# Performance work log

Measured on AMD Instinct MI355X. Metric: run time of the kernel, lower is better.

Reference implementation:

```python
import jax, jax.numpy as jnp
import numpy as np
from jax import lax

# ---- constants matching init_kwargs ----
NY, NX = 1024, 1024
DX, DY = 50.0, 50.0
TTOT = 32.0
DTMAX = 0.5
RHO, G, FD = 910.0, 9.81, 1e-17
EPS = 1e-10
T_FREQ = 5.0
N_STEPS = 64            # fixed step count (>= TTOT/DTMAX); dt masked to 0 once time >= TTOT
LAPSE = 0.0065          # degC per m elevation lapse rate (SMB model)
MELT_FACTOR = 0.5       # m ice / (degC * yr) ablation factor (SMB model)


def update_smb(Z_surf, precip, T_ma_lowest, T_mj_lowest, ice_mask):
    # Lapse-rate temperatures at the surface
    T_ma = T_ma_lowest - LAPSE * Z_surf   # mean annual temperature
    T_mj = T_mj_lowest - LAPSE * Z_surf   # mean July temperature
    accumulation = precip * (T_ma < 0.0).astype(Z_surf.dtype)
    ablation = MELT_FACTOR * jnp.maximum(T_mj, 0.0)
    return (accumulation - ablation) * ice_mask


def setup_inputs() -> dict:
    key = jax.random.key(0)
    k1, k2, k3 = jax.random.split(key, 3)
    # smooth mountain topography: 2500 m gaussian massif + small noise
    y = np.arange(NY, dtype=np.float32) * DY
    x = np.arange(NX, dtype=np.float32) * DX
    yy, xx = np.meshgrid(y, x, indexing="ij")
    cy, cx = y.mean(), x.mean()
    sigma = 0.25 * NX * DX
    z = 2500.0 * np.exp(-((yy - cy) ** 2 + (xx - cx) ** 2) / (2.0 * sigma ** 2))
    Z_topo = jnp.asarray(z, dtype=jnp.float32) + 5.0 * jax.random.normal(k1, (NY, NX), dtype=jnp.float32)
    precip_tensor = 2.0 * jax.random.uniform(k2, (NY, NX), dtype=jnp.float32)  # m ice / yr
    T_ma_lowest = jnp.float32(8.0) + jax.random.normal(k3, (), dtype=jnp.float32)
    T_mj_lowest = T_ma_lowest + jnp.float32(8.0)
    ice_mask = jnp.ones((NY, NX), dtype=jnp.float32)
    return {"precip_tensor": precip_tensor, "T_ma_lowest": T_ma_lowest,
            "T_mj_lowest": T_mj_lowest, "Z_topo": Z_topo, "ice_mask": ice_mask}


def _glacier_step(carry, _, Z_topo, precip, T_ma_lowest, T_mj_lowest, ice_mask):
    H_ice, Z_surf, smb, time, t_last = carry
    # staggered-grid averages and slopes (SIA diffusion)
    H_avg = 0.25 * (H_ice[:-1, :-1] + H_ice[1:, 1:] + H_ice[:-1, 1:] + H_ice[1:, :-1])
    Sx = (Z_surf[:, 1:] - Z_surf[:, :-1]) / DX
    Sy = (Z_surf[1:, :] - Z_surf[:-1, :]) / DY
    Sx = 0.5 * (Sx[:-1, :] + Sx[1:, :])          # (NY-1, NX-1)
    Sy = 0.5 * (Sy[:, :-1] + Sy[:, 1:])          # (NY-1, NX-1)
    Snorm = jnp.sqrt(Sx ** 2 + Sy ** 2 + EPS)
    D = FD * (RHO * G) ** 3 * H_avg ** 5 * Snorm ** 2 + EPS
    # adaptive CFL dt; torch uses .item() so dt is a non-differentiable constant
    dt = jnp.minimum(min(DX, DY) ** 2 / (2.7 * jnp.max(D)), DTMAX)
    dt = lax.stop_gradient(dt)
    dt = jnp.where(time < TTOT, dt, 0.0)         # freeze once ttot is reached
    qx = -(0.5 * (D[:-1, :] + D[1:, :])) * (Z_surf[1:-1, 1:] - Z_surf[1:-1, :-1]) / DX
    qy = -(0.5 * (D[:, :-1] + D[:, 1:])) * (Z_surf[1:, 1:-1] - Z_surf[:-1, 1:-1]) / DY
    dHdt = -(jnp.diff(qx, axis=1) / DX + jnp.diff(qy, axis=0) / DY)  # (NY-2, NX-2)
    H_new = H_ice.at[1:-1, 1:-1].add(dt * (dHdt + smb[1:-1, 1:-1]))
    H_new = jnp.maximum(H_new, 0.0)
    Z_new = Z_topo + H_new
    time = time + dt
    # refresh SMB every T_FREQ model years
    do_upd = (time - t_last) >= T_FREQ
    smb_new = update_smb(Z_new, precip, T_ma_lowest, T_mj_lowest, ice_mask)
    smb = jnp.where(do_upd, smb_new, smb)
    t_last = jnp.where(do_upd, time, t_last)
    return (H_new, Z_new, smb, time, t_last), None


def reference(precip_tensor, T_ma_lowest, T_mj_lowest, Z_topo, ice_mask):
    H_ice = jnp.zeros((NY, NX), dtype=jnp.float32)
    Z_surf = Z_topo + H_ice
    smb = update_smb(Z_surf, precip_tensor, T_ma_lowest, T_mj_lowest, ice_mask)
    time = jnp.float32(0.0)
    t_last = jnp.float32(0.0)
    step = lambda c, x: _glacier_step(c, x, Z_topo, precip_tensor, T_ma_lowest, T_mj_lowest, ice_mask)
    (H_ice, _, _, _, _), _ = lax.scan(step, (H_ice, Z_surf, smb, time, t_last), None, length=N_STEPS)
    return H_ice
```

## Files before the change

kernel.cpp:

```cpp
#include <hip/hip_runtime.h>
#include <math.h>

#define NYg 1024
#define NXg 1024
#define W   1024
#define NSTEPS 64
#define NBLK 256
#define EN (NBLK * W)

#define WS_SLOTS 0
#define WS_NBF   24576
#define WS_CTRL_END 32768
#define WS_GRIDS 32768

constexpr float DXf   = 50.0f;
constexpr float DYf   = 50.0f;
constexpr float TTOTf = 32.0f;
constexpr float DTMAXf= 0.5f;
constexpr float EPSf  = 1e-10f;
constexpr float TFREQ = 5.0f;
constexpr float LAPSE = 0.0065f;
constexpr float MELTF = 0.5f;
constexpr double RHOG = 910.0 * 9.81;
constexpr float  CDf  = (float)(1e-17 * RHOG * RHOG * RHOG);

__device__ __forceinline__ float scloadf(const float* p) {
    return __hip_atomic_load(p, __ATOMIC_RELAXED, __HIP_MEMORY_SCOPE_SYSTEM);
}
__device__ __forceinline__ void scstoref(float* p, float v) {
    __hip_atomic_store(p, v, __ATOMIC_RELAXED, __HIP_MEMORY_SCOPE_SYSTEM);
}
__device__ __forceinline__ unsigned scloadu(const unsigned* p) {
    return __hip_atomic_load(p, __ATOMIC_RELAXED, __HIP_MEMORY_SCOPE_SYSTEM);
}

__device__ __forceinline__ float dfunc(float h00, float h01, float h10, float h11,
                                       float z00, float z01, float z10, float z11)
{
    float havg = 0.25f * (h00 + h11 + h01 + h10);
    float sx = ((z01 - z00) + (z11 - z10)) * (0.5f / DXf);
    float sy = ((z10 - z00) + (z11 - z01)) * (0.5f / DYf);
    float sn = sqrtf(sx * sx + sy * sy + EPSf);
    float h2 = havg * havg;
    float h4 = h2 * h2;
    return CDf * (h4 * havg) * (sn * sn) + EPSf;
}

__global__ __launch_bounds__(256) void k_init(unsigned* __restrict__ ctrl)
{
    int idx = blockIdx.x * blockDim.x + threadIdx.x;
    int stride = gridDim.x * blockDim.x;
    for (int i = idx; i < WS_CTRL_END; i += stride) {
        unsigned v = 0u;
        if (i < NBLK) v = __float_as_uint(EPSf);
        ctrl[i] = v;
    }
}

__global__ __launch_bounds__(1024, 1) void k_run(
    float* __restrict__ EZa0, float* __restrict__ EZa1,
    float* __restrict__ EZb0, float* __restrict__ EZb1,
    float* __restrict__ EDa0, float* __restrict__ EDa1,
    float* __restrict__ EDb0, float* __restrict__ EDb1,
    const float* __restrict__ ztopo, const float* __restrict__ precip,
    const float* __restrict__ mask, const float* __restrict__ tma,
    const float* __restrict__ tmj, unsigned* __restrict__ ctrl,
    float* __restrict__ Hout)
{
    __shared__ float sZ[5][W];
    __shared__ float sH[5][W];
    __shared__ float sD[4][W];
    __shared__ float smax16[16];
    __shared__ float smax4[4];

    float*    slotsf = (float*)ctrl;
    unsigned* nbf    = ctrl + WS_NBF;

    const int c   = threadIdx.x;
    const int b   = blockIdx.x;
    const int r0  = b * 4;
    const int lane = c & 63, wid = c >> 6;
    const bool hasA = (b > 0), hasB = (b < NBLK - 1);
    const bool cL = (c >= 1), cR = (c <= NXg - 2);
    const int cm = (c == 0) ? 0 : c - 1;
    const int cp = (c == W - 1) ? W - 1 : c + 1;

    const float TMA = tma[0], TMJ = tmj[0];

    float z_[7];
    float h_[5];
    float dreg[4];
    float dtop, dtopL;
    float dbot, dbotL;
    float smbr[5], ztr[5];

    #pragma unroll
    for (int q = 0; q < 7; ++q) {
        int r = r0 - 1 + q;
        z_[q] = (r >= 0 && r < NYg) ? ztopo[r * W + c] : 0.0f;
    }
    #pragma unroll
    for (int rr = 0; rr < 5; ++rr) {
        int r = r0 + rr;
        h_[rr] = 0.0f;
        if (r < NYg) {
            float z = z_[rr + 1];
            ztr[rr] = z;
            float t_ma = TMA - LAPSE * z;
            float t_mj = TMJ - LAPSE * z;
            float acc  = (t_ma < 0.0f) ? precip[r * W + c] : 0.0f;
            float abl  = MELTF * fmaxf(t_mj, 0.0f);
            smbr[rr] = (acc - abl) * mask[r * W + c];
            sZ[rr][c] = z;
            sH[rr][c] = 0.0f;
        } else {
            ztr[rr] = 0.0f; smbr[rr] = 0.0f;
            sZ[rr][c] = 0.0f;
            sH[rr][c] = 0.0f;
        }
    }
    dtop = EPSf; dtopL = EPSf; dbot = EPSf; dbotL = EPSf;
    #pragma unroll
    for (int q = 0; q < 4; ++q) { dreg[q] = EPSf; sD[q][c] = EPSf; }
    __syncthreads();

    float t = 0.0f, tl = 0.0f;

    for (int s = 0; s < NSTEPS; ++s) {
        const float* EZar = (s & 1) ? EZa1 : EZa0;
        float*       EZaw = (s & 1) ? EZa0 : EZa1;
        const float* EZbr = (s & 1) ? EZb1 : EZb0;
        float*       EZbw = (s & 1) ? EZb0 : EZb1;
        const float* EDar = (s & 1) ? EDa1 : EDa0;
        float*       EDaw = (s & 1) ? EDa0 : EDa1;
        const float* EDbr = (s & 1) ? EDb1 : EDb0;
        float*       EDbw = (s & 1) ? EDb0 : EDb1;

        if (s > 0) {
            if (hasA)
                while (scloadu(&nbf[(b - 1) * 32]) < (unsigned)s) __builtin_amdgcn_s_sleep(1);
            if (hasB)
                while (scloadu(&nbf[(b + 1) * 32]) < (unsigned)s) __builtin_amdgcn_s_sleep(1);
            if (hasA) {
                z_[0] = scloadf(EZbr + (b - 1) * W + c);
                if (cR) dtop  = scloadf(EDbr + (b - 1) * W + c);
                if (cL) dtopL = scloadf(EDbr + (b - 1) * W + (c-1));
            }
            if (hasB) {
                z_[6] = scloadf(EZar + (b + 1) * W + c);
                if (cR) dbot  = scloadf(EDar + (b + 1) * W + c);
                if (cL) dbotL = scloadf(EDar + (b + 1) * W + (c-1));
            }
        }

        float dl[6], doa[6];
        dl[0] = dtopL;      doa[0] = dtop;
        dl[1] = sD[0][cm];  doa[1] = dreg[0];
        dl[2] = sD[1][cm];  doa[2] = dreg[1];
        dl[3] = sD[2][cm];  doa[3] = dreg[2];
        dl[4] = sD[3][cm];  doa[4] = dreg[3];
        dl[5] = dbotL;      doa[5] = dbot;

        float zl[5], zr[5];
        #pragma unroll
        for (int q = 0; q < 5; ++q) { zl[q] = sZ[q][cm]; zr[q] = sZ[q][cp]; }

        float qy[6];
        #pragma unroll
        for (int k = 0; k < 6; ++k)
            qy[k] = -0.5f * (dl[k] + doa[k]) * (z_[k + 1] - z_[k]) * (1.0f / DYf);

        float dh[5];
        bool  inter[5];
        #pragma unroll
        for (int rr = 0; rr < 5; ++rr) {
            int r = r0 + rr;
            bool iv = (r >= 1 && r <= NYg - 2 && cL && cR);
            float zc  = z_[rr + 1];
            float qxR = -0.5f * (doa[rr] + doa[rr + 1]) * (zr[rr] - zc) * (1.0f / DXf);
            float qxL = -0.5f * (dl[rr]  + dl[rr + 1])  * (zc - zl[rr]) * (1.0f / DXf);
            float d = -((qxR - qxL) * (1.0f / DXf) + (qy[rr + 1] - qy[rr]) * (1.0f / DYf));
            dh[rr] = iv ? d : 0.0f;
            inter[rr] = iv;
        }

        if (c < NBLK) {
            const float* sl = slotsf + s * NBLK + c;
            float v = scloadf(sl);
            while (__float_as_uint(v) == 0u) { __builtin_amdgcn_s_sleep(1); v = scloadf(sl); }
            #pragma unroll
            for (int off = 32; off >= 1; off >>= 1)
                v = fmaxf(v, __shfl_xor(v, off, 64));
            if (lane == 0) smax4[wid] = v;
        }
        __syncthreads();

        float mD = fmaxf(fmaxf(smax4[0], smax4[1]), fmaxf(smax4[2], smax4[3]));
        float dt = fminf(2500.0f / (2.7f * mD), DTMAXf);
        if (!(t < TTOTf)) dt = 0.0f;
        float nt  = t + dt;
        bool  upd = (nt - tl) >= TFREQ;

        #pragma unroll
        for (int rr = 0; rr < 5; ++rr) {
            int r = r0 + rr;
            if (r < NYg) {
                float h, z;
                if (inter[rr]) { h = fmaxf(h_[rr] + dt * (dh[rr] + smbr[rr]), 0.0f);
                                 z = ztr[rr] + h; }
                else           { h = 0.0f; z = z_[rr + 1]; }
                h_[rr] = h; z_[rr + 1] = z;
                sZ[rr][c] = z;
                sH[rr][c] = h;
                if (rr == 1 && hasA) scstoref(EZaw + b * W + c, z);
                if (rr == 3 && hasB) scstoref(EZbw + b * W + c, z);
                if (upd) {
                    float t_ma = TMA - LAPSE * z;
                    float t_mj = TMJ - LAPSE * z;
                    float acc  = (t_ma < 0.0f) ? precip[r * W + c] : 0.0f;
                    float abl  = MELTF * fmaxf(t_mj, 0.0f);
                    smbr[rr] = (acc - abl) * mask[r * W + c];
                }
            } else {
                h_[rr] = 0.0f;
            }
        }
        __syncthreads();

        if (s < NSTEPS - 1) {
            float m = 0.0f;
            float dv[4];
            #pragma unroll
            for (int rr = 0; rr < 4; ++rr) {
                int i = r0 + rr;
                float dd = 0.0f;
                if (i <= NYg - 2 && cR) {
                    dd = dfunc(h_[rr], sH[rr][c + 1],
                               h_[rr + 1], sH[rr + 1][c + 1],
                               z_[rr + 1], sZ[rr][c + 1],
                               z_[rr + 2], sZ[rr + 1][c + 1]);
                    m = fmaxf(m, dd);
                    if (rr == 0 && hasA) scstoref(EDaw + b * W + c, dd);
                    if (rr == 3 && hasB) scstoref(EDbw + b * W + c, dd);
                }
                dv[rr] = dd;
            }
            sD[0][c] = dv[0];
            sD[1][c] = dv[1];
            sD[2][c] = dv[2];
            sD[3][c] = dv[3];
            dreg[0] = dv[0]; dreg[1] = dv[1]; dreg[2] = dv[2]; dreg[3] = dv[3];
            #pragma unroll
            for (int off = 32; off >= 1; off >>= 1)
                m = fmaxf(m, __shfl_xor(m, off, 64));
            if (lane == 0) smax16[wid] = m;
            __syncthreads();
            if (c == 0) {
                #pragma unroll
                for (int q = 1; q < 16; ++q) m = fmaxf(m, smax16[q]);
                scstoref(slotsf + (s + 1) * NBLK + b, m);
            }
            asm volatile("s_waitcnt vmcnt(0)" ::: "memory");
            __syncthreads();
            if (c == 0)
                __hip_atomic_store(&nbf[b * 32], (unsigned)(s + 1),
                                   __ATOMIC_RELAXED, __HIP_MEMORY_SCOPE_SYSTEM);
        }

        t = nt;
        if (upd) tl = nt;
    }

    #pragma unroll
    for (int rr = 0; rr < 4; ++rr)
        Hout[(r0 + rr) * W + c] = h_[rr];
}

extern "C" void kernel_launch(void* const* d_in, const int* in_sizes, int n_in,
                              void* d_out, int out_size, void* d_ws, size_t ws_size,
                              hipStream_t stream)
{
    const float* precip = (const float*)d_in[0];
    const float* tma    = (const float*)d_in[1];
    const float* tmj    = (const float*)d_in[2];
    const float* ztopo  = (const float*)d_in[3];
    const float* mask   = (const float*)d_in[4];

    unsigned* ctrl = (unsigned*)d_ws;
    float* g = (float*)d_ws + WS_GRIDS;
    float* EZa0 = g + 0 * EN; float* EZa1 = g + 1 * EN;
    float* EZb0 = g + 2 * EN; float* EZb1 = g + 3 * EN;
    float* EDa0 = g + 4 * EN; float* EDa1 = g + 5 * EN;
    float* EDb0 = g + 6 * EN; float* EDb1 = g + 7 * EN;

    k_init<<<dim3(64), dim3(256), 0, stream>>>(ctrl);

    k_run<<<dim3(256), dim3(1024), 0, stream>>>(EZa0, EZa1, EZb0, EZb1,
                                                EDa0, EDa1, EDb0, EDb1,
                                                ztopo, precip, mask, tma, tmj,
                                                ctrl, (float*)d_out);
}
```

Measured before the change: 392.6 us.

## Speculate dt equals DTMAX to overlap update with global max reduction wait

Each step now computes the H/Z update and the next diffusivity using a guessed dt (DTMAX, or zero past TTOT) before waiting on the cross-block max slots. Once the true dt is known, it recomputes only if the guess was wrong, then commits state and publishes the block max. This hides the spin-wait latency behind useful work when the CFL limit is not active. It costs extra registers and duplicated code, and a full recompute on mispredicted steps.

```diff
diff --git a/kernel.cpp b/kernel.cpp
--- a/kernel.cpp
+++ b/kernel.cpp
@@ -184,49 +184,30 @@
             inter[rr] = iv;
         }
 
-        if (c < NBLK) {
-            const float* sl = slotsf + s * NBLK + c;
-            float v = scloadf(sl);
-            while (__float_as_uint(v) == 0u) { __builtin_amdgcn_s_sleep(1); v = scloadf(sl); }
-            #pragma unroll
-            for (int off = 32; off >= 1; off >>= 1)
-                v = fmaxf(v, __shfl_xor(v, off, 64));
-            if (lane == 0) smax4[wid] = v;
-        }
         __syncthreads();
 
-        float mD = fmaxf(fmaxf(smax4[0], smax4[1]), fmaxf(smax4[2], smax4[3]));
-        float dt = fminf(2500.0f / (2.7f * mD), DTMAXf);
-        if (!(t < TTOTf)) dt = 0.0f;
-        float nt  = t + dt;
-        bool  upd = (nt - tl) >= TFREQ;
-
+        const float dtg = (t < TTOTf) ? DTMAXf : 0.0f;
+        float hs[5], zs[5];
         #pragma unroll
         for (int rr = 0; rr < 5; ++rr) {
             int r = r0 + rr;
             if (r < NYg) {
                 float h, z;
-                if (inter[rr]) { h = fmaxf(h_[rr] + dt * (dh[rr] + smbr[rr]), 0.0f);
+                if (inter[rr]) { h = fmaxf(h_[rr] + dtg * (dh[rr] + smbr[rr]), 0.0f);
                                  z = ztr[rr] + h; }
                 else           { h = 0.0f; z = z_[rr + 1]; }
-                h_[rr] = h; z_[rr + 1] = z;
+                hs[rr] = h; zs[rr] = z;
                 sZ[rr][c] = z;
                 sH[rr][c] = h;
                 if (rr == 1 && hasA) scstoref(EZaw + b * W + c, z);
                 if (rr == 3 && hasB) scstoref(EZbw + b * W + c, z);
-                if (upd) {
-                    float t_ma = TMA - LAPSE * z;
-                    float t_mj = TMJ - LAPSE * z;
-                    float acc  = (t_ma < 0.0f) ? precip[r * W + c] : 0.0f;
-                    float abl  = MELTF * fmaxf(t_mj, 0.0f);
-                    smbr[rr] = (acc - abl) * mask[r * W + c];
-                }
             } else {
-                h_[rr] = 0.0f;
+                hs[rr] = 0.0f; zs[rr] = z_[rr + 1];
             }
         }
         __syncthreads();
 
+        float m16 = 0.0f;
         if (s < NSTEPS - 1) {
             float m = 0.0f;
             float dv[4];
@@ -235,10 +216,10 @@
                 int i = r0 + rr;
                 float dd = 0.0f;
                 if (i <= NYg - 2 && cR) {
-                    dd = dfunc(h_[rr], sH[rr][c + 1],
-                               h_[rr + 1], sH[rr + 1][c + 1],
-                               z_[rr + 1], sZ[rr][c + 1],
-                               z_[rr + 2], sZ[rr + 1][c + 1]);
+                    dd = dfunc(hs[rr], sH[rr][c + 1],
+                               hs[rr + 1], sH[rr + 1][c + 1],
+                               zs[rr], sZ[rr][c + 1],
+                               zs[rr + 1], sZ[rr + 1][c + 1]);
                     m = fmaxf(m, dd);
                     if (rr == 0 && hasA) scstoref(EDaw + b * W + c, dd);
                     if (rr == 3 && hasB) scstoref(EDbw + b * W + c, dd);
@@ -258,8 +239,98 @@
             if (c == 0) {
                 #pragma unroll
                 for (int q = 1; q < 16; ++q) m = fmaxf(m, smax16[q]);
-                scstoref(slotsf + (s + 1) * NBLK + b, m);
-            }
+                m16 = m;
+            }
+        }
+
+        if (c < NBLK) {
+            const float* sl = slotsf + s * NBLK + c;
+            float v = scloadf(sl);
+            while (__float_as_uint(v) == 0u) { __builtin_amdgcn_s_sleep(1); v = scloadf(sl); }
+            #pragma unroll
+            for (int off = 32; off >= 1; off >>= 1)
+                v = fmaxf(v, __shfl_xor(v, off, 64));
+            if (lane == 0) smax4[wid] = v;
+        }
+        __syncthreads();
+
+        float mD = fmaxf(fmaxf(smax4[0], smax4[1]), fmaxf(smax4[2], smax4[3]));
+        float dt = fminf(2500.0f / (2.7f * mD), DTMAXf);
+        if (!(t < TTOTf)) dt = 0.0f;
+
+        if (__float_as_uint(dt) != __float_as_uint(dtg)) {
+            #pragma unroll
+            for (int rr = 0; rr < 5; ++rr) {
+                int r = r0 + rr;
+                if (r < NYg) {
+                    float h, z;
+                    if (inter[rr]) { h = fmaxf(h_[rr] + dt * (dh[rr] + smbr[rr]), 0.0f);
+                                     z = ztr[rr] + h; }
+                    else           { h = 0.0f; z = z_[rr + 1]; }
+                    hs[rr] = h; zs[rr] = z;
+                    sZ[rr][c] = z;
+                    sH[rr][c] = h;
+                    if (rr == 1 && hasA) scstoref(EZaw + b * W + c, z);
+                    if (rr == 3 && hasB) scstoref(EZbw + b * W + c, z);
+                }
+            }
+            __syncthreads();
+            if (s < NSTEPS - 1) {
+                float m = 0.0f;
+                float dv[4];
+                #pragma unroll
+                for (int rr = 0; rr < 4; ++rr) {
+                    int i = r0 + rr;
+                    float dd = 0.0f;
+                    if (i <= NYg - 2 && cR) {
+                        dd = dfunc(hs[rr], sH[rr][c + 1],
+                                   hs[rr + 1], sH[rr + 1][c + 1],
+                                   zs[rr], sZ[rr][c + 1],
+                                   zs[rr + 1], sZ[rr + 1][c + 1]);
+                        m = fmaxf(m, dd);
+                        if (rr == 0 && hasA) scstoref(EDaw + b * W + c, dd);
+                        if (rr == 3 && hasB) scstoref(EDbw + b * W + c, dd);
+                    }
+                    dv[rr] = dd;
+                }
+                sD[0][c] = dv[0];
+                sD[1][c] = dv[1];
+                sD[2][c] = dv[2];
+                sD[3][c] = dv[3];
+                dreg[0] = dv[0]; dreg[1] = dv[1]; dreg[2] = dv[2]; dreg[3] = dv[3];
+                #pragma unroll
+                for (int off = 32; off >= 1; off >>= 1)
+                    m = fmaxf(m, __shfl_xor(m, off, 64));
+                if (lane == 0) smax16[wid] = m;
+                __syncthreads();
+                if (c == 0) {
+                    #pragma unroll
+                    for (int q = 1; q < 16; ++q) m = fmaxf(m, smax16[q]);
+                    m16 = m;
+                }
+            }
+        }
+
+        float nt  = t + dt;
+        bool  upd = (nt - tl) >= TFREQ;
+        #pragma unroll
+        for (int rr = 0; rr < 5; ++rr) {
+            h_[rr] = hs[rr];
+            z_[rr + 1] = zs[rr];
+            int r = r0 + rr;
+            if (upd && r < NYg) {
+                float z = zs[rr];
+                float t_ma = TMA - LAPSE * z;
+                float t_mj = TMJ - LAPSE * z;
+                float acc  = (t_ma < 0.0f) ? precip[r * W + c] : 0.0f;
+                float abl  = MELTF * fmaxf(t_mj, 0.0f);
+                smbr[rr] = (acc - abl) * mask[r * W + c];
+            }
+        }
+
+        if (s < NSTEPS - 1) {
+            if (c == 0)
+                scstoref(slotsf + (s + 1) * NBLK + b, m16);
             asm volatile("s_waitcnt vmcnt(0)" ::: "memory");
             __syncthreads();
             if (c == 0)
```

Result: no change. 393.3 us (+0.2%).

## Split grid into 512 persistent blocks of two rows each

Applied to the files above, without the earlier changes.

The persistent stencil kernel now uses 512 blocks that each own two rows, instead of 256 blocks owning four rows. The aim is two co-resident blocks per CU, which doubles wave occupancy for latency hiding and halves per-block work on each step's critical path. Halo exchange now uses one shared Z-row buffer plus separate up and down D buffers, and the global max reduction reads 512 slots. In exchange it relies on all 512 blocks being resident at once, because of the spin-wait neighbour flags. The launch bound of 8 also tightens the register budget, which may cause spills.

```diff
diff --git a/kernel.cpp b/kernel.cpp
--- a/kernel.cpp
+++ b/kernel.cpp
@@ -5,13 +5,12 @@
 #define NXg 1024
 #define W   1024
 #define NSTEPS 64
-#define NBLK 256
+#define NBLK 512
 #define EN (NBLK * W)
 
-#define WS_SLOTS 0
-#define WS_NBF   24576
-#define WS_CTRL_END 32768
-#define WS_GRIDS 32768
+#define WS_NBF   33280
+#define WS_CTRL_END 49664
+#define WS_GRIDS 65536
 
 constexpr float DXf   = 50.0f;
 constexpr float DYf   = 50.0f;
@@ -57,28 +56,27 @@
     }
 }
 
-__global__ __launch_bounds__(1024, 1) void k_run(
-    float* __restrict__ EZa0, float* __restrict__ EZa1,
-    float* __restrict__ EZb0, float* __restrict__ EZb1,
-    float* __restrict__ EDa0, float* __restrict__ EDa1,
-    float* __restrict__ EDb0, float* __restrict__ EDb1,
+__global__ __launch_bounds__(1024, 8) void k_run(
+    float* __restrict__ EZ0,  float* __restrict__ EZ1,
+    float* __restrict__ EDd0, float* __restrict__ EDd1,
+    float* __restrict__ EDu0, float* __restrict__ EDu1,
     const float* __restrict__ ztopo, const float* __restrict__ precip,
     const float* __restrict__ mask, const float* __restrict__ tma,
     const float* __restrict__ tmj, unsigned* __restrict__ ctrl,
     float* __restrict__ Hout)
 {
-    __shared__ float sZ[5][W];
-    __shared__ float sH[5][W];
-    __shared__ float sD[4][W];
+    __shared__ float sZ[3][W];
+    __shared__ float sH[3][W];
+    __shared__ float sD[2][W];
     __shared__ float smax16[16];
-    __shared__ float smax4[4];
+    __shared__ float smax8[8];
 
     float*    slotsf = (float*)ctrl;
     unsigned* nbf    = ctrl + WS_NBF;
 
     const int c   = threadIdx.x;
     const int b   = blockIdx.x;
-    const int r0  = b * 4;
+    const int r0  = b * 2;
     const int lane = c & 63, wid = c >> 6;
     const bool hasA = (b > 0), hasB = (b < NBLK - 1);
     const bool cL = (c >= 1), cR = (c <= NXg - 2);
@@ -87,20 +85,20 @@
 
     const float TMA = tma[0], TMJ = tmj[0];
 
-    float z_[7];
-    float h_[5];
-    float dreg[4];
+    float z_[5];
+    float h_[3];
+    float dreg[2];
     float dtop, dtopL;
     float dbot, dbotL;
-    float smbr[5], ztr[5];
-
-    #pragma unroll
-    for (int q = 0; q < 7; ++q) {
+    float smbr[3], ztr[3];
+
+    #pragma unroll
+    for (int q = 0; q < 5; ++q) {
         int r = r0 - 1 + q;
         z_[q] = (r >= 0 && r < NYg) ? ztopo[r * W + c] : 0.0f;
     }
     #pragma unroll
-    for (int rr = 0; rr < 5; ++rr) {
+    for (int rr = 0; rr < 3; ++rr) {
         int r = r0 + rr;
         h_[rr] = 0.0f;
         if (r < NYg) {
@@ -121,20 +119,18 @@
     }
     dtop = EPSf; dtopL = EPSf; dbot = EPSf; dbotL = EPSf;
     #pragma unroll
-    for (int q = 0; q < 4; ++q) { dreg[q] = EPSf; sD[q][c] = EPSf; }
+    for (int q = 0; q < 2; ++q) { dreg[q] = EPSf; sD[q][c] = EPSf; }
     __syncthreads();
 
     float t = 0.0f, tl = 0.0f;
 
     for (int s = 0; s < NSTEPS; ++s) {
-        const float* EZar = (s & 1) ? EZa1 : EZa0;
-        float*       EZaw = (s & 1) ? EZa0 : EZa1;
-        const float* EZbr = (s & 1) ? EZb1 : EZb0;
-        float*       EZbw = (s & 1) ? EZb0 : EZb1;
-        const float* EDar = (s & 1) ? EDa1 : EDa0;
-        float*       EDaw = (s & 1) ? EDa0 : EDa1;
-        const float* EDbr = (s & 1) ? EDb1 : EDb0;
-        float*       EDbw = (s & 1) ? EDb0 : EDb1;
+        const float* EZr  = (s & 1) ? EZ1  : EZ0;
+        float*       EZw  = (s & 1) ? EZ0  : EZ1;
+        const float* EDdr = (s & 1) ? EDd1 : EDd0;
+        float*       EDdw = (s & 1) ? EDd0 : EDd1;
+        const float* EDur = (s & 1) ? EDu1 : EDu0;
+        float*       EDuw = (s & 1) ? EDu0 : EDu1;
 
         if (s > 0) {
             if (hasA)
@@ -142,38 +138,36 @@
             if (hasB)
                 while (scloadu(&nbf[(b + 1) * 32]) < (unsigned)s) __builtin_amdgcn_s_sleep(1);
             if (hasA) {
-                z_[0] = scloadf(EZbr + (b - 1) * W + c);
-                if (cR) dtop  = scloadf(EDbr + (b - 1) * W + c);
-                if (cL) dtopL = scloadf(EDbr + (b - 1) * W + (c-1));
+                z_[0] = scloadf(EZr + (b - 1) * W + c);
+                if (cR) dtop  = scloadf(EDur + (b - 1) * W + c);
+                if (cL) dtopL = scloadf(EDur + (b - 1) * W + (c-1));
             }
             if (hasB) {
-                z_[6] = scloadf(EZar + (b + 1) * W + c);
-                if (cR) dbot  = scloadf(EDar + (b + 1) * W + c);
-                if (cL) dbotL = scloadf(EDar + (b + 1) * W + (c-1));
-            }
-        }
-
-        float dl[6], doa[6];
+                z_[4] = scloadf(EZr + (b + 1) * W + c);
+                if (cR) dbot  = scloadf(EDdr + (b + 1) * W + c);
+                if (cL) dbotL = scloadf(EDdr + (b + 1) * W + (c-1));
+            }
+        }
+
+        float dl[4], doa[4];
         dl[0] = dtopL;      doa[0] = dtop;
         dl[1] = sD[0][cm];  doa[1] = dreg[0];
         dl[2] = sD[1][cm];  doa[2] = dreg[1];
-        dl[3] = sD[2][cm];  doa[3] = dreg[2];
-        dl[4] = sD[3][cm];  doa[4] = dreg[3];
-        dl[5] = dbotL;      doa[5] = dbot;
-
-        float zl[5], zr[5];
-        #pragma unroll
-        for (int q = 0; q < 5; ++q) { zl[q] = sZ[q][cm]; zr[q] = sZ[q][cp]; }
-
-        float qy[6];
-        #pragma unroll
-        for (int k = 0; k < 6; ++k)
+        dl[3] = dbotL;      doa[3] = dbot;
+
+        float zl[3], zr[3];
+        #pragma unroll
+        for (int q = 0; q < 3; ++q) { zl[q] = sZ[q][cm]; zr[q] = sZ[q][cp]; }
+
+        float qy[4];
+        #pragma unroll
+        for (int k = 0; k < 4; ++k)
             qy[k] = -0.5f * (dl[k] + doa[k]) * (z_[k + 1] - z_[k]) * (1.0f / DYf);
 
-        float dh[5];
-        bool  inter[5];
-        #pragma unroll
-        for (int rr = 0; rr < 5; ++rr) {
+        float dh[3];
+        bool  inter[3];
+        #pragma unroll
+        for (int rr = 0; rr < 3; ++rr) {
             int r = r0 + rr;
             bool iv = (r >= 1 && r <= NYg - 2 && cL && cR);
             float zc  = z_[rr + 1];
@@ -191,18 +185,19 @@
             #pragma unroll
             for (int off = 32; off >= 1; off >>= 1)
                 v = fmaxf(v, __shfl_xor(v, off, 64));
-            if (lane == 0) smax4[wid] = v;
+            if (lane == 0) smax8[wid] = v;
         }
         __syncthreads();
 
-        float mD = fmaxf(fmaxf(smax4[0], smax4[1]), fmaxf(smax4[2], smax4[3]));
+        float mD = fmaxf(fmaxf(fmaxf(smax8[0], smax8[1]), fmaxf(smax8[2], smax8[3])),
+                         fmaxf(fmaxf(smax8[4], smax8[5]), fmaxf(smax8[6], smax8[7])));
         float dt = fminf(2500.0f / (2.7f * mD), DTMAXf);
         if (!(t < TTOTf)) dt = 0.0f;
         float nt  = t + dt;
         bool  upd = (nt - tl) >= TFREQ;
 
         #pragma unroll
-        for (int rr = 0; rr < 5; ++rr) {
+        for (int rr = 0; rr < 3; ++rr) {
             int r = r0 + rr;
             if (r < NYg) {
                 float h, z;
@@ -212,8 +207,7 @@
                 h_[rr] = h; z_[rr + 1] = z;
                 sZ[rr][c] = z;
                 sH[rr][c] = h;
-                if (rr == 1 && hasA) scstoref(EZaw + b * W + c, z);
-                if (rr == 3 && hasB) scstoref(EZbw + b * W + c, z);
+                if (rr == 1) scstoref(EZw + b * W + c, z);
                 if (upd) {
                     float t_ma = TMA - LAPSE * z;
                     float t_mj = TMJ - LAPSE * z;
@@ -229,27 +223,22 @@
 
         if (s < NSTEPS - 1) {
             float m = 0.0f;
-            float dv[4];
-            #pragma unroll
-            for (int rr = 0; rr < 4; ++rr) {
-                int i = r0 + rr;
-                float dd = 0.0f;
-                if (i <= NYg - 2 && cR) {
-                    dd = dfunc(h_[rr], sH[rr][c + 1],
-                               h_[rr + 1], sH[rr + 1][c + 1],
-                               z_[rr + 1], sZ[rr][c + 1],
-                               z_[rr + 2], sZ[rr + 1][c + 1]);
-                    m = fmaxf(m, dd);
-                    if (rr == 0 && hasA) scstoref(EDaw + b * W + c, dd);
-                    if (rr == 3 && hasB) scstoref(EDbw + b * W + c, dd);
-                }
-                dv[rr] = dd;
-            }
-            sD[0][c] = dv[0];
-            sD[1][c] = dv[1];
-            sD[2][c] = dv[2];
-            sD[3][c] = dv[3];
-            dreg[0] = dv[0]; dreg[1] = dv[1]; dreg[2] = dv[2]; dreg[3] = dv[3];
+            float dv0 = 0.0f, dv1 = 0.0f;
+            if (cR) {
+                dv0 = dfunc(h_[0], sH[0][c + 1], h_[1], sH[1][c + 1],
+                            z_[1], sZ[0][c + 1], z_[2], sZ[1][c + 1]);
+                m = fmaxf(m, dv0);
+                if (hasA) scstoref(EDdw + b * W + c, dv0);
+            }
+            if (r0 + 1 <= NYg - 2 && cR) {
+                dv1 = dfunc(h_[1], sH[1][c + 1], h_[2], sH[2][c + 1],
+                            z_[2], sZ[1][c + 1], z_[3], sZ[2][c + 1]);
+                m = fmaxf(m, dv1);
+                if (hasB) scstoref(EDuw + b * W + c, dv1);
+            }
+            sD[0][c] = dv0;
+            sD[1][c] = dv1;
+            dreg[0] = dv0; dreg[1] = dv1;
             #pragma unroll
             for (int off = 32; off >= 1; off >>= 1)
                 m = fmaxf(m, __shfl_xor(m, off, 64));
@@ -272,7 +261,7 @@
     }
 
     #pragma unroll
-    for (int rr = 0; rr < 4; ++rr)
+    for (int rr = 0; rr < 2; ++rr)
         Hout[(r0 + rr) * W + c] = h_[rr];
 }
 
@@ -288,15 +277,13 @@
 
     unsigned* ctrl = (unsigned*)d_ws;
     float* g = (float*)d_ws + WS_GRIDS;
-    float* EZa0 = g + 0 * EN; float* EZa1 = g + 1 * EN;
-    float* EZb0 = g + 2 * EN; float* EZb1 = g + 3 * EN;
-    float* EDa0 = g + 4 * EN; float* EDa1 = g + 5 * EN;
-    float* EDb0 = g + 6 * EN; float* EDb1 = g + 7 * EN;
+    float* EZ0  = g + 0 * EN; float* EZ1  = g + 1 * EN;
+    float* EDd0 = g + 2 * EN; float* EDd1 = g + 3 * EN;
+    float* EDu0 = g + 4 * EN; float* EDu1 = g + 5 * EN;
 
     k_init<<<dim3(64), dim3(256), 0, stream>>>(ctrl);
 
-    k_run<<<dim3(256), dim3(1024), 0, stream>>>(EZa0, EZa1, EZb0, EZb1,
-                                                EDa0, EDa1, EDb0, EDb1,
+    k_run<<<dim3(512), dim3(1024), 0, stream>>>(EZ0, EZ1, EDd0, EDd1, EDu0, EDu1,
                                                 ztopo, precip, mask, tma, tmj,
                                                 ctrl, (float*)d_out);
 }
```

New measurement: 643.4 us. 63.9% more time.
